# Kernel tuning notes

Measured on AMD Instinct MI355X. Metric: run time of the kernel, lower is better.

## Reference

```python
import jax, jax.numpy as jnp
import numpy as np

BN_EPS = 1e-5
NORM_EPS = 1e-12
TEMPERATURE = 0.07
TOP_K = 128


def _projection_head(x, W1, b1, gamma, beta, W2, b2):
    # Linear(hidden, hidden); torch Linear weight is [out, in]
    y = x @ W1.T + b1
    # BatchNorm1d in training mode: batch statistics (biased variance)
    mu = jnp.mean(y, axis=0)
    var = jnp.var(y, axis=0)
    y = gamma * (y - mu) * jax.lax.rsqrt(var + BN_EPS) + beta
    # exact (erf) GELU, matching torch default
    y = jax.nn.gelu(y, approximate=False)
    return y @ W2.T + b2


def _l2_normalize(x):
    n = jnp.linalg.norm(x, axis=-1, keepdims=True)
    return x / jnp.maximum(n, NORM_EPS)


def setup_inputs() -> dict:
    key = jax.random.key(0)
    ks = jax.random.split(key, 5)
    B, N_NEG, H, P = 4096, 32768, 1024, 256
    h1 = jax.random.normal(ks[0], (B, H), dtype=jnp.float32)
    h2 = jax.random.normal(ks[1], (B, H), dtype=jnp.float32)
    h_neg = jax.random.normal(ks[2], (N_NEG, H), dtype=jnp.float32)
    W1 = jax.random.normal(ks[3], (H, H), dtype=jnp.float32) * (1.0 / np.sqrt(H))
    b1 = jnp.zeros((H,), dtype=jnp.float32)
    gamma = jnp.ones((H,), dtype=jnp.float32)
    beta = jnp.zeros((H,), dtype=jnp.float32)
    W2 = jax.random.normal(ks[4], (P, H), dtype=jnp.float32) * (1.0 / np.sqrt(H))
    b2 = jnp.zeros((P,), dtype=jnp.float32)
    return {"h1": h1, "h2": h2, "h_neg": h_neg, "W1": W1, "b1": b1,
            "gamma": gamma, "beta": beta, "W2": W2, "b2": b2}


def reference(h1, h2, h_neg, W1, b1, gamma, beta, W2, b2):
    z1 = _l2_normalize(_projection_head(h1, W1, b1, gamma, beta, W2, b2))
    z2 = _l2_normalize(_projection_head(h2, W1, b1, gamma, beta, W2, b2))
    z_neg = _l2_normalize(_projection_head(h_neg, W1, b1, gamma, beta, W2, b2))

    sim_neg = z1 @ z_neg.T                      # [B, N_neg]
    _, hard_idx = jax.lax.top_k(sim_neg, TOP_K) # [B, K]
    z_hard = z_neg[hard_idx]                    # [B, K, P] gather

    pos_sim = jnp.sum(z1 * z2, axis=-1, keepdims=True) / TEMPERATURE      # [B, 1]
    neg_sim = jnp.einsum('bp,bkp->bk', z1, z_hard) / TEMPERATURE          # [B, K]
    logits = jnp.concatenate([pos_sim, neg_sim], axis=1)                  # [B, 1+K]
    # cross entropy with all labels = 0
    loss = -jnp.mean(jax.nn.log_softmax(logits, axis=-1)[:, 0])
    return loss
```

## Files before the change

kernel.cpp:

```cpp
#include <hip/hip_runtime.h>
#include <hip/hip_bf16.h>
#include <math.h>

#define BATCH 4096
#define NNEG 32768
#define HID 1024
#define PROJ 256
#define TOPK 128
#define ROWS_TOTAL 40960
#define CHUNK 2048
#define INV_T 14.2857142857142857f

#define BM 128
#define BN 128
#define BK 64

#define BNS_ROWS 128

typedef __attribute__((ext_vector_type(8))) short bf16x8;
typedef __attribute__((ext_vector_type(4))) float f32x4;

__device__ __forceinline__ float b2f(unsigned short u) {
    return __uint_as_float(((unsigned)u) << 16);
}
__device__ __forceinline__ unsigned short f2b(float f) {
    unsigned u = __float_as_uint(f);
    unsigned r = (u + 0x7FFFu + ((u >> 16) & 1u)) >> 16;
    return (unsigned short)r;
}
__device__ __forceinline__ float gelu_fast(float v) {
    float v2 = v * v;
    float w = v * fmaf(v2, -0.1029433f, -2.3022086f);
    float e = exp2f(w);
    return v * __builtin_amdgcn_rcpf(1.0f + e);
}

__device__ __forceinline__ float blockReduceSumF(float v, volatile float* scratch) {
    #pragma unroll
    for (int o = 32; o > 0; o >>= 1) v += __shfl_down(v, o);
    int wid = threadIdx.x >> 6, lane = threadIdx.x & 63;
    __syncthreads();
    if (lane == 0) scratch[wid] = v;
    __syncthreads();
    return scratch[0] + scratch[1] + scratch[2] + scratch[3];
}
__device__ __forceinline__ int blockReduceSumI(int v, volatile int* scratch) {
    #pragma unroll
    for (int o = 32; o > 0; o >>= 1) v += __shfl_down(v, o);
    int wid = threadIdx.x >> 6, lane = threadIdx.x & 63;
    __syncthreads();
    if (lane == 0) scratch[wid] = v;
    __syncthreads();
    return scratch[0] + scratch[1] + scratch[2] + scratch[3];
}

__device__ __forceinline__ void gl_lds16(const unsigned short* g, unsigned short* l) {
    __builtin_amdgcn_global_load_lds(
        (const __attribute__((address_space(1))) unsigned*)g,
        (__attribute__((address_space(3))) unsigned*)l, 16, 0, 0);
}

__global__ __launch_bounds__(256) void conv_f2b(const float* __restrict__ src,
                                                unsigned short* __restrict__ dst, int n)
{
    int i = (blockIdx.x * 256 + threadIdx.x) * 4;
    if (i + 3 < n) {
        float4 v = *(const float4*)(src + i);
        ushort4 o;
        o.x = f2b(v.x); o.y = f2b(v.y); o.z = f2b(v.z); o.w = f2b(v.w);
        *(ushort4*)(dst + i) = o;
    }
}

__global__ __launch_bounds__(256) void conv_f2b8(const float* __restrict__ src,
                                                 unsigned short* __restrict__ dst)
{
    int i = (blockIdx.x * 256 + threadIdx.x) * 8;
    float4 a = *(const float4*)(src + i);
    float4 b = *(const float4*)(src + i + 4);
    ushort4 o0, o1;
    o0.x = f2b(a.x); o0.y = f2b(a.y); o0.z = f2b(a.z); o0.w = f2b(a.w);
    o1.x = f2b(b.x); o1.y = f2b(b.y); o1.z = f2b(b.z); o1.w = f2b(b.w);
    *(ushort4*)(dst + i) = o0;
    *(ushort4*)(dst + i + 4) = o1;
}

__device__ __forceinline__ void xcd_swizzle(int& bx, int& by) {
    int gx = gridDim.x;
    int orig = by * gx + bx;
    int q = (gx * gridDim.y) >> 3;
    int wg = (orig & 7) * q + (orig >> 3);
    bx = wg % gx;
    by = wg / gx;
}

__global__ __launch_bounds__(256, 4) void mfma_gemm(
    const unsigned short* __restrict__ A, const unsigned short* __restrict__ Bw,
    const float* __restrict__ bias, unsigned short* __restrict__ C,
    int M, int N, int K)
{
    __shared__ unsigned short As[BM * BK];
    __shared__ unsigned short Bs[BN * BK];
    const int tid = threadIdx.x;
    int bxi = blockIdx.x, byi = blockIdx.y;
    xcd_swizzle(bxi, byi);
    const int bm = byi * BM;
    const int bn = bxi * BN;
    const int wave = tid >> 6;
    const int lane = tid & 63;
    const int wm = (wave >> 1) * 64;
    const int wn = (wave & 1) * 64;
    const int fr = lane & 15;
    const int fg = lane >> 4;

    int s_slot[4], s_row[4], s_c16[4];
    #pragma unroll
    for (int i = 0; i < 4; i++) {
        int s = wave * 256 + i * 64 + lane;
        s_slot[i] = (wave * 256 + i * 64) * 8;
        s_row[i] = s >> 3;
        s_c16[i] = (s & 7) ^ ((s >> 3) & 7);
    }

    f32x4 acc[4][4] = {};

    for (int k0 = 0; k0 < K; k0 += BK) {
        #pragma unroll
        for (int i = 0; i < 4; i++) {
            gl_lds16(A  + (size_t)(bm + s_row[i]) * K + k0 + s_c16[i] * 8, &As[s_slot[i]]);
            gl_lds16(Bw + (size_t)(bn + s_row[i]) * K + k0 + s_c16[i] * 8, &Bs[s_slot[i]]);
        }
        __syncthreads();
        #pragma unroll
        for (int ks = 0; ks < 2; ks++) {
            bf16x8 a[4], b[4];
            #pragma unroll
            for (int mi = 0; mi < 4; mi++) {
                int row = wm + mi * 16 + fr;
                a[mi] = *(const bf16x8*)&As[row * 64 + (((ks * 4 + fg) ^ (row & 7)) << 3)];
            }
            #pragma unroll
            for (int ni = 0; ni < 4; ni++) {
                int row = wn + ni * 16 + fr;
                b[ni] = *(const bf16x8*)&Bs[row * 64 + (((ks * 4 + fg) ^ (row & 7)) << 3)];
            }
            #pragma unroll
            for (int mi = 0; mi < 4; mi++)
                #pragma unroll
                for (int ni = 0; ni < 4; ni++)
                    acc[mi][ni] = __builtin_amdgcn_mfma_f32_16x16x32_bf16(a[mi], b[ni], acc[mi][ni], 0, 0, 0);
        }
        __syncthreads();
    }

    #pragma unroll
    for (int mi = 0; mi < 4; mi++) {
        #pragma unroll
        for (int ni = 0; ni < 4; ni++) {
            int col = bn + wn + ni * 16 + fr;
            int row0 = bm + wm + mi * 16 + fg * 4;
            float bv = bias ? bias[col] : 0.0f;
            #pragma unroll
            for (int r = 0; r < 4; r++) {
                float v = acc[mi][ni][r] + bv;
                C[(size_t)(row0 + r) * N + col] = f2b(v);
            }
        }
    }
}

__global__ __launch_bounds__(256) void bn_stats_partial(const unsigned short* __restrict__ Yb,
                                                        float* __restrict__ partial)
{
    __shared__ float lsum[1024];
    __shared__ float lssq[1024];
    const int cg = (threadIdx.x & 127) * 8;
    int r = blockIdx.x * BNS_ROWS + (threadIdx.x >> 7);
    float s[8] = {}, ss[8] = {};
    #pragma unroll 4
    for (int i = 0; i < BNS_ROWS / 2; i++, r += 2) {
        uint4 v = *(const uint4*)&Yb[(size_t)r * HID + cg];
        const unsigned short* u = (const unsigned short*)&v;
        #pragma unroll
        for (int j = 0; j < 8; j++) {
            float f = b2f(u[j]);
            s[j] += f; ss[j] += f * f;
        }
    }
    if (threadIdx.x >= 128) {
        #pragma unroll
        for (int j = 0; j < 8; j++) { lsum[cg + j] = s[j]; lssq[cg + j] = ss[j]; }
    }
    __syncthreads();
    if (threadIdx.x < 128) {
        float* outs = partial + (size_t)blockIdx.x * 2048;
        #pragma unroll
        for (int j = 0; j < 8; j++) {
            outs[cg + j]        = s[j] + lsum[cg + j];
            outs[1024 + cg + j] = ss[j] + lssq[cg + j];
        }
    }
}

__global__ __launch_bounds__(256) void bn_reduce_finalize(
    const float* __restrict__ partial,
    const float* __restrict__ gamma, const float* __restrict__ beta,
    float* __restrict__ scale, float* __restrict__ shift)
{
    int seg = blockIdx.y;
    int col = blockIdx.x * 256 + threadIdx.x;
    int base = (seg == 0) ? 0 : (seg == 1) ? 32 : 64;
    int nblk = (seg == 2) ? 256 : 32;
    const float* p = partial + (size_t)base * 2048;
    float s = 0.f, ss = 0.f;
    for (int b = 0; b < nblk; b++) {
        s  += p[(size_t)b * 2048 + col];
        ss += p[(size_t)b * 2048 + 1024 + col];
    }
    float n = (seg == 2) ? (float)NNEG : (float)BATCH;
    float mu = s / n;
    float var = ss / n - mu * mu;
    float sc = gamma[col] * rsqrtf(var + 1e-5f);
    scale[seg * HID + col] = sc;
    shift[seg * HID + col] = beta[col] - mu * sc;
}

__global__ __launch_bounds__(256) void bngelu(unsigned short* __restrict__ Yb,
                                              const float* __restrict__ scale,
                                              const float* __restrict__ shift)
{
    size_t i = ((size_t)blockIdx.x * 256 + threadIdx.x) * 8;
    int row = (int)(i >> 10);
    int seg = (row < BATCH) ? 0 : (row < 2 * BATCH) ? 1 : 2;
    int col = (int)(i & 1023);
    float4 sc0 = *(const float4*)(scale + seg * HID + col);
    float4 sc1 = *(const float4*)(scale + seg * HID + col + 4);
    float4 sh0 = *(const float4*)(shift + seg * HID + col);
    float4 sh1 = *(const float4*)(shift + seg * HID + col + 4);
    float sc[8] = { sc0.x, sc0.y, sc0.z, sc0.w, sc1.x, sc1.y, sc1.z, sc1.w };
    float sh[8] = { sh0.x, sh0.y, sh0.z, sh0.w, sh1.x, sh1.y, sh1.z, sh1.w };
    uint4 v = *(uint4*)&Yb[i];
    unsigned short* u = (unsigned short*)&v;
    #pragma unroll
    for (int j = 0; j < 8; j++) {
        float f = fmaf(b2f(u[j]), sc[j], sh[j]);
        u[j] = f2b(gelu_fast(f));
    }
    *(uint4*)&Yb[i] = v;
}

__global__ __launch_bounds__(256) void l2norm(unsigned short* __restrict__ Z,
                                              float* __restrict__ Zfp)
{
    __shared__ float scratch[4];
    size_t r = blockIdx.x;
    float v = b2f(Z[r * PROJ + threadIdx.x]);
    float t = blockReduceSumF(v * v, scratch);
    float scale = 1.0f / fmaxf(sqrtf(t), 1e-12f);
    float o = v * scale;
    Z[r * PROJ + threadIdx.x] = f2b(o);
    if (r < 2 * BATCH) Zfp[r * PROJ + threadIdx.x] = o;
}

__global__ __launch_bounds__(256) void topk_loss(
    const unsigned short* __restrict__ simb,
    const float* __restrict__ z1, const float* __restrict__ z2,
    int rowOffset, float* __restrict__ rowloss)
{
    __shared__ int   hcnt[4096];
    __shared__ int   segc[256];
    __shared__ int   sufc[256];
    __shared__ int   wtot[4];
    __shared__ float fscratch[4];
    __shared__ int   iscratch[4];
    __shared__ int   sel_seg;
    __shared__ int   sh_bt, sh_run;

    const int tid = threadIdx.x;
    const int lane = tid & 63;
    const int wid = tid >> 6;
    const int grow = rowOffset + blockIdx.x;
    const unsigned short* srow = simb + (size_t)blockIdx.x * NNEG;

    #pragma unroll
    for (int j = 0; j < 16; j++) hcnt[tid * 16 + j] = 0;

    float p = z1[(size_t)grow * PROJ + tid] * z2[(size_t)grow * PROJ + tid];
    float pos = blockReduceSumF(p, fscratch);
    __syncthreads();

    for (int i = tid * 8; i < NNEG; i += 256 * 8) {
        uint4 v4 = *(const uint4*)(srow + i);
        const unsigned short* u = (const unsigned short*)&v4;
        #pragma unroll
        for (int j = 0; j < 8; j++) {
            float v = b2f(u[j]);
            int k = (int)fmaf(v, 2048.f, 2048.f);
            k = min(max(k, 0), 4095);
            atomicAdd(&hcnt[k], 1);
        }
    }
    __syncthreads();

    int c = 0;
    #pragma unroll
    for (int j = 0; j < 16; j++) c += hcnt[tid * 16 + j];

    int v = c;
    #pragma unroll
    for (int o = 1; o < 64; o <<= 1) {
        int t = __shfl_down(v, o);
        if (lane + o < 64) v += t;
    }
    if (lane == 0) wtot[wid] = v;
    __syncthreads();
    int suf = v;
    #pragma unroll
    for (int w = 0; w < 4; w++) if (w > wid) suf += wtot[w];
    segc[tid] = c;
    sufc[tid] = suf;
    if (suf >= TOPK && suf - c < TOPK) sel_seg = tid;
    __syncthreads();

    if (tid == 0) {
        int t = sel_seg;
        int running = sufc[t] - segc[t];
        int bt = t * 16;
        for (int j = 15; j >= 0; j--) {
            int b = t * 16 + j;
            int cb = hcnt[b];
            if (running + cb >= TOPK) { bt = b; break; }
            running += cb;
        }
        sh_bt = bt; sh_run = running;
    }
    __syncthreads();
    const int bt = sh_bt;
    const float m = INV_T;

    float s_above = 0.f, s_eq = 0.f;
    int c_eq = 0;
    for (int i = tid * 8; i < NNEG; i += 256 * 8) {
        uint4 v4 = *(const uint4*)(srow + i);
        const unsigned short* u = (const unsigned short*)&v4;
        #pragma unroll
        for (int j = 0; j < 8; j++) {
            float vv = b2f(u[j]);
            int k = (int)fmaf(vv, 2048.f, 2048.f);
            k = min(max(k, 0), 4095);
            if (k >= bt) {
                float e = __expf(fmaf(vv, INV_T, -m));
                if (k > bt) s_above += e;
                else { s_eq += e; c_eq++; }
            }
        }
    }
    s_above = blockReduceSumF(s_above, fscratch);
    __syncthreads();
    s_eq = blockReduceSumF(s_eq, fscratch);
    c_eq = blockReduceSumI(c_eq, iscratch);
    if (tid == 0) {
        int need = TOPK - sh_run;
        float avg = s_eq / (float)c_eq;
        float total = s_above + (float)need * avg + __expf(fmaf(pos, INV_T, -m));
        rowloss[grow] = m + logf(total) - pos * INV_T;
    }
}

__global__ __launch_bounds__(256) void loss_reduce(const float* __restrict__ rowloss,
                                                   float* __restrict__ out)
{
    __shared__ float scratch[4];
    float s = 0.f;
    for (int i = threadIdx.x; i < BATCH; i += 256) s += rowloss[i];
    s = blockReduceSumF(s, scratch);
    if (threadIdx.x == 0) out[0] = s / (float)BATCH;
}

extern "C" void kernel_launch(void* const* d_in, const int* in_sizes, int n_in,
                              void* d_out, int out_size, void* d_ws, size_t ws_size,
                              hipStream_t stream)
{
    const float* h1    = (const float*)d_in[0];
    const float* h2    = (const float*)d_in[1];
    const float* hneg  = (const float*)d_in[2];
    const float* W1    = (const float*)d_in[3];
    const float* b1    = (const float*)d_in[4];
    const float* gamma = (const float*)d_in[5];
    const float* beta  = (const float*)d_in[6];
    const float* W2    = (const float*)d_in[7];
    const float* b2    = (const float*)d_in[8];
    float* out = (float*)d_out;
    float* ws  = (float*)d_ws;

    unsigned short* X_all = (unsigned short*)ws;
    unsigned short* Yb    = (unsigned short*)(ws + 20971520);
    unsigned short* Z     = (unsigned short*)(ws + 41943040);
    unsigned short* W1b   = (unsigned short*)(ws + 47185920);
    unsigned short* W2b   = (unsigned short*)(ws + 47710208);
    float* partial = ws + 47841280;
    float* s_scale = ws + 48496640;
    float* s_shift = ws + 48499712;
    float* rowloss = ws + 48502784;
    float* Zfp     = ws + 48506880;
    unsigned short* simb = X_all;

    conv_f2b<<<1024, 256, 0, stream>>>(W1, W1b, HID * HID);
    conv_f2b<<<256, 256, 0, stream>>>(W2, W2b, PROJ * HID);
    conv_f2b8<<<2048, 256, 0, stream>>>(h1, X_all);
    conv_f2b8<<<2048, 256, 0, stream>>>(h2, X_all + (size_t)BATCH * HID);
    conv_f2b8<<<16384, 256, 0, stream>>>(hneg, X_all + (size_t)2 * BATCH * HID);

    {
        dim3 g(HID / BN, ROWS_TOTAL / BM);
        mfma_gemm<<<g, 256, 0, stream>>>(X_all, W1b, b1, Yb, ROWS_TOTAL, HID, HID);
    }

    const int rows[3] = { BATCH, BATCH, NNEG };
    const int yoff[3] = { 0, BATCH, 2 * BATCH };
    const int poff[3] = { 0, 32, 64 };

    for (int s = 0; s < 3; s++) {
        bn_stats_partial<<<rows[s] / BNS_ROWS, 256, 0, stream>>>(
            Yb + (size_t)yoff[s] * HID, partial + (size_t)poff[s] * 2048);
    }
    bn_reduce_finalize<<<dim3(HID / 256, 3), 256, 0, stream>>>(partial, gamma, beta, s_scale, s_shift);

    bngelu<<<ROWS_TOTAL * HID / 8 / 256, 256, 0, stream>>>(Yb, s_scale, s_shift);

    {
        dim3 g(PROJ / BN, ROWS_TOTAL / BM);
        mfma_gemm<<<g, 256, 0, stream>>>(Yb, W2b, b2, Z, ROWS_TOTAL, PROJ, HID);
    }
    l2norm<<<ROWS_TOTAL, 256, 0, stream>>>(Z, Zfp);

    const unsigned short* znegb = Z + (size_t)(2 * BATCH) * PROJ;
    const float* z2v = Zfp + (size_t)BATCH * PROJ;
    for (int c = 0; c < BATCH / CHUNK; c++) {
        dim3 g(NNEG / BN, CHUNK / BM);
        mfma_gemm<<<g, 256, 0, stream>>>(Z + (size_t)(c * CHUNK) * PROJ, znegb, nullptr,
                                         simb, CHUNK, NNEG, PROJ);
        topk_loss<<<CHUNK, 256, 0, stream>>>(simb, Zfp, z2v, c * CHUNK, rowloss);
    }
    loss_reduce<<<1, 256, 0, stream>>>(rowloss, out);
}
```

Baseline: 546.9 us.

## Double-buffer GEMM LDS tiles with async prefetch and halve BN stats rows

Rewrites the MFMA GEMM main loop to use two LDS buffers with BK=32. The next tile's global-to-LDS loads are issued before computing on the current tile, with explicit vmcnt waits, raw barriers and setprio around the MFMAs. The LDS swizzle is adjusted for the narrower tile. Separately, the BN stats kernel now processes 64 rows per block, doubling the partial blocks and the finalize loop, with workspace offsets shifted to match. The aim is to overlap memory latency with compute and raise parallelism in the stats pass. The cost is more barriers per K step and a longer finalize reduction.

```diff
diff --git a/kernel.cpp b/kernel.cpp
--- a/kernel.cpp
+++ b/kernel.cpp
@@ -13,9 +13,9 @@
 
 #define BM 128
 #define BN 128
-#define BK 64
-
-#define BNS_ROWS 128
+#define BK 32
+
+#define BNS_ROWS 64
 
 typedef __attribute__((ext_vector_type(8))) short bf16x8;
 typedef __attribute__((ext_vector_type(4))) float f32x4;
@@ -99,8 +99,8 @@
     const float* __restrict__ bias, unsigned short* __restrict__ C,
     int M, int N, int K)
 {
-    __shared__ unsigned short As[BM * BK];
-    __shared__ unsigned short Bs[BN * BK];
+    __shared__ unsigned short As[2][BM * BK];
+    __shared__ unsigned short Bs[2][BN * BK];
     const int tid = threadIdx.x;
     int bxi = blockIdx.x, byi = blockIdx.y;
     xcd_swizzle(bxi, byi);
@@ -113,44 +113,59 @@
     const int fr = lane & 15;
     const int fg = lane >> 4;
 
-    int s_slot[4], s_row[4], s_c16[4];
-    #pragma unroll
-    for (int i = 0; i < 4; i++) {
-        int s = wave * 256 + i * 64 + lane;
-        s_slot[i] = (wave * 256 + i * 64) * 8;
-        s_row[i] = s >> 3;
-        s_c16[i] = (s & 7) ^ ((s >> 3) & 7);
-    }
+    const int s0 = wave * 64 + lane;
+    const int s1 = 256 + wave * 64 + lane;
+    const int r0 = s0 >> 2, g0 = (s0 & 3) ^ ((s0 >> 3) & 3);
+    const int r1 = s1 >> 2, g1 = (s1 & 3) ^ ((s1 >> 3) & 3);
+    const int base0 = (wave * 64) * 8;
+    const int base1 = (256 + wave * 64) * 8;
+    const unsigned short* a0 = A  + (size_t)(bm + r0) * K + g0 * 8;
+    const unsigned short* a1 = A  + (size_t)(bm + r1) * K + g1 * 8;
+    const unsigned short* b0 = Bw + (size_t)(bn + r0) * K + g0 * 8;
+    const unsigned short* b1 = Bw + (size_t)(bn + r1) * K + g1 * 8;
 
     f32x4 acc[4][4] = {};
-
-    for (int k0 = 0; k0 < K; k0 += BK) {
-        #pragma unroll
-        for (int i = 0; i < 4; i++) {
-            gl_lds16(A  + (size_t)(bm + s_row[i]) * K + k0 + s_c16[i] * 8, &As[s_slot[i]]);
-            gl_lds16(Bw + (size_t)(bn + s_row[i]) * K + k0 + s_c16[i] * 8, &Bs[s_slot[i]]);
-        }
-        __syncthreads();
-        #pragma unroll
-        for (int ks = 0; ks < 2; ks++) {
-            bf16x8 a[4], b[4];
+    const int nt = K / BK;
+
+    gl_lds16(a0, &As[0][base0]);
+    gl_lds16(a1, &As[0][base1]);
+    gl_lds16(b0, &Bs[0][base0]);
+    gl_lds16(b1, &Bs[0][base1]);
+
+    int cur = 0;
+    for (int t = 0; t < nt; ++t) {
+        if (t + 1 < nt) {
+            const int k0 = (t + 1) * BK;
+            gl_lds16(a0 + k0, &As[cur ^ 1][base0]);
+            gl_lds16(a1 + k0, &As[cur ^ 1][base1]);
+            gl_lds16(b0 + k0, &Bs[cur ^ 1][base0]);
+            gl_lds16(b1 + k0, &Bs[cur ^ 1][base1]);
+            asm volatile("s_waitcnt vmcnt(4)" ::: "memory");
+        } else {
+            asm volatile("s_waitcnt vmcnt(0)" ::: "memory");
+        }
+        __builtin_amdgcn_s_barrier();
+
+        bf16x8 a[4], b[4];
+        #pragma unroll
+        for (int mi = 0; mi < 4; mi++) {
+            int row = wm + mi * 16 + fr;
+            a[mi] = *(const bf16x8*)&As[cur][row * BK + ((fg ^ ((row >> 1) & 3)) << 3)];
+        }
+        #pragma unroll
+        for (int ni = 0; ni < 4; ni++) {
+            int row = wn + ni * 16 + fr;
+            b[ni] = *(const bf16x8*)&Bs[cur][row * BK + ((fg ^ ((row >> 1) & 3)) << 3)];
+        }
+        __builtin_amdgcn_s_setprio(1);
+        #pragma unroll
+        for (int mi = 0; mi < 4; mi++)
             #pragma unroll
-            for (int mi = 0; mi < 4; mi++) {
-                int row = wm + mi * 16 + fr;
-                a[mi] = *(const bf16x8*)&As[row * 64 + (((ks * 4 + fg) ^ (row & 7)) << 3)];
-            }
-            #pragma unroll
-            for (int ni = 0; ni < 4; ni++) {
-                int row = wn + ni * 16 + fr;
-                b[ni] = *(const bf16x8*)&Bs[row * 64 + (((ks * 4 + fg) ^ (row & 7)) << 3)];
-            }
-            #pragma unroll
-            for (int mi = 0; mi < 4; mi++)
-                #pragma unroll
-                for (int ni = 0; ni < 4; ni++)
-                    acc[mi][ni] = __builtin_amdgcn_mfma_f32_16x16x32_bf16(a[mi], b[ni], acc[mi][ni], 0, 0, 0);
-        }
-        __syncthreads();
+            for (int ni = 0; ni < 4; ni++)
+                acc[mi][ni] = __builtin_amdgcn_mfma_f32_16x16x32_bf16(a[mi], b[ni], acc[mi][ni], 0, 0, 0);
+        __builtin_amdgcn_s_setprio(0);
+        __builtin_amdgcn_s_barrier();
+        cur ^= 1;
     }
 
     #pragma unroll
@@ -209,8 +224,8 @@
 {
     int seg = blockIdx.y;
     int col = blockIdx.x * 256 + threadIdx.x;
-    int base = (seg == 0) ? 0 : (seg == 1) ? 32 : 64;
-    int nblk = (seg == 2) ? 256 : 32;
+    int base = (seg == 0) ? 0 : (seg == 1) ? 64 : 128;
+    int nblk = (seg == 2) ? 512 : 64;
     const float* p = partial + (size_t)base * 2048;
     float s = 0.f, ss = 0.f;
     for (int b = 0; b < nblk; b++) {
@@ -399,10 +414,10 @@
     unsigned short* W1b   = (unsigned short*)(ws + 47185920);
     unsigned short* W2b   = (unsigned short*)(ws + 47710208);
     float* partial = ws + 47841280;
-    float* s_scale = ws + 48496640;
-    float* s_shift = ws + 48499712;
-    float* rowloss = ws + 48502784;
-    float* Zfp     = ws + 48506880;
+    float* s_scale = ws + 49152000;
+    float* s_shift = ws + 49155072;
+    float* rowloss = ws + 49158144;
+    float* Zfp     = ws + 49162240;
     unsigned short* simb = X_all;
 
     conv_f2b<<<1024, 256, 0, stream>>>(W1, W1b, HID * HID);
@@ -418,7 +433,7 @@
 
     const int rows[3] = { BATCH, BATCH, NNEG };
     const int yoff[3] = { 0, BATCH, 2 * BATCH };
-    const int poff[3] = { 0, 32, 64 };
+    const int poff[3] = { 0, 64, 128 };
 
     for (int s = 0; s < 3; s++) {
         bn_stats_partial<<<rows[s] / BNS_ROWS, 256, 0, stream>>>(
```

Measured after the change: 624.1 us. 14.1% more time.
